# Kernel tuning notes

Measured on AMD Instinct MI355X. Metric: run time of the kernel, lower is better.

## Reference

```python
import jax, jax.numpy as jnp
import numpy as np

B, N, NKV = 2, 2048, 2048
E = 4096
H = 16
HD = E // H          # 256 head_dim
LQ = E // 8          # 512 q latent
LKV = E // 16        # 256 kv latent


def setup_inputs() -> dict:
    key = jax.random.key(0)
    ks = jax.random.split(key, 6)
    Q = jax.random.normal(ks[0], (B, N, E), dtype=jnp.float32)
    K = jax.random.normal(ks[1], (B, NKV, E), dtype=jnp.float32)
    # Linear weights stored as (in, out); scaled ~1/sqrt(fan_in) like torch default init
    Wq_d = jax.random.normal(ks[2], (E, LQ), dtype=jnp.float32) / np.sqrt(E)
    W_qk = jax.random.normal(ks[3], (LQ, H * LKV), dtype=jnp.float32) / np.sqrt(LQ)
    Wkv_d = jax.random.normal(ks[4], (E, LKV), dtype=jnp.float32) / np.sqrt(E)
    Wv_u = jax.random.normal(ks[5], (LKV, H * HD), dtype=jnp.float32) / np.sqrt(LKV)
    return {"Q": Q, "K": K, "Wq_d": Wq_d, "W_qk": W_qk, "Wkv_d": Wkv_d, "Wv_u": Wv_u}


def reference(Q, K, Wq_d, W_qk, Wkv_d, Wv_u):
    b, n, _ = Q.shape
    nkv = K.shape[1]
    C_q = Q @ Wq_d                                   # [B,N,Lq]
    C_kv = K @ Wkv_d                                 # [B,Nkv,Lkv]
    CqWqk = (C_q @ W_qk).reshape(b, n, H, LKV)       # [B,N,H,Lkv]
    # scores contract over the kv latent dim (absorbed-weight MLA)
    scores = jnp.einsum('bnhl,bkl->bhnk', CqWqk, C_kv) / jnp.sqrt(
        jnp.asarray(LKV, dtype=Q.dtype))             # [B,H,N,Nkv]
    attn = jax.nn.softmax(scores, axis=-1)
    V_up = (C_kv @ Wv_u).reshape(b, nkv, H, HD)      # [B,Nkv,H,hd]
    out = jnp.einsum('bhnk,bkhd->bnhd', attn, V_up)  # [B,N,H,hd]
    return out.reshape(b, n, H * HD)                 # [B,N,E]
```

## Files before the change

kernel.cpp:

```cpp
#include <hip/hip_runtime.h>


#define B_ 2
#define N_ 2048
#define H_ 16
#define HD_ 256
#define LKV_ 256

typedef __attribute__((ext_vector_type(8))) short bf8;
typedef __attribute__((ext_vector_type(4))) float f4;
typedef __attribute__((ext_vector_type(4))) unsigned short us4v;
typedef unsigned short u16;

__device__ __forceinline__ u16 f2b(float f) {
  union { float f; unsigned u; } v; v.f = f;
  unsigned r = (v.u + 0x7FFFu + ((v.u >> 16) & 1u)) >> 16;
  return (u16)r;
}

__device__ __forceinline__ void load_lds16(const void* g, void* l) {
  __builtin_amdgcn_global_load_lds(
      (const __attribute__((address_space(1))) unsigned int*)(unsigned long long)(uintptr_t)g,
      (__attribute__((address_space(3))) unsigned int*)(unsigned int)(uintptr_t)l,
      16, 0, 0);
}

__global__ __launch_bounds__(256) void cvt_bf16(const float* __restrict__ src,
                                                u16* __restrict__ dst, int n4)
{
  int i = blockIdx.x * 256 + threadIdx.x;
  if (i < n4) {
    float4 v = *(const float4*)(src + (size_t)i * 4);
    us4v o = {f2b(v.x), f2b(v.y), f2b(v.z), f2b(v.w)};
    *(us4v*)(dst + (size_t)i * 4) = o;
  }
}

__global__ __launch_bounds__(256) void cvt_transpose(const float* __restrict__ src,
                                                     u16* __restrict__ dst, int R, int C)
{
  __shared__ float tile[32][33];
  const int t = threadIdx.x;
  const int tr = t & 31, tc = t >> 5;
  const int r0 = blockIdx.x * 32, c0 = blockIdx.y * 32;
#pragma unroll
  for (int i = 0; i < 4; ++i)
    tile[tc + i * 8][tr] = src[(size_t)(r0 + tc + i * 8) * C + c0 + tr];
  __syncthreads();
#pragma unroll
  for (int i = 0; i < 4; ++i)
    dst[(size_t)(c0 + tc + i * 8) * R + r0 + tr] = f2b(tile[tr][tc + i * 8]);
}

__global__ __launch_bounds__(256) void gemm_bt(
    const u16* __restrict__ A,
    const u16* __restrict__ Bt,
    u16* __restrict__ C,
    int M, int N, int K)
{
  __shared__ u16 As[128 * 32];
  __shared__ u16 Bs[128 * 32];

  const int t = threadIdx.x;
  const int w = t >> 6, lane = t & 63;
  const int quad = lane >> 4, l16 = lane & 15;
  const int n0 = blockIdx.x * 128, m0 = blockIdx.y * 128;
  const int wm = (w >> 1) * 64, wn = (w & 1) * 64;

  f4 acc[4][4];
#pragma unroll
  for (int mi = 0; mi < 4; ++mi)
#pragma unroll
    for (int ni = 0; ni < 4; ++ni) acc[mi][ni] = (f4){0.f, 0.f, 0.f, 0.f};

  const u16* Ap = A + (size_t)m0 * K;
  const u16* Bp = Bt + (size_t)n0 * K;
  const int srow = t >> 2, spos = (t & 3) * 8;

  for (int k0 = 0; k0 < K; k0 += 32) {
    __syncthreads();
    load_lds16(Ap + (size_t)srow * K + k0 + spos,        &As[(size_t)t * 8]);
    load_lds16(Ap + (size_t)(srow + 64) * K + k0 + spos, &As[(size_t)(256 + t) * 8]);
    load_lds16(Bp + (size_t)srow * K + k0 + spos,        &Bs[(size_t)t * 8]);
    load_lds16(Bp + (size_t)(srow + 64) * K + k0 + spos, &Bs[(size_t)(256 + t) * 8]);
    __syncthreads();

    bf8 af[4], bfr[4];
#pragma unroll
    for (int mi = 0; mi < 4; ++mi)
      af[mi] = *(const bf8*)(&As[(wm + mi * 16 + l16) * 32 + quad * 8]);
#pragma unroll
    for (int ni = 0; ni < 4; ++ni)
      bfr[ni] = *(const bf8*)(&Bs[(wn + ni * 16 + l16) * 32 + quad * 8]);
#pragma unroll
    for (int mi = 0; mi < 4; ++mi)
#pragma unroll
      for (int ni = 0; ni < 4; ++ni)
        acc[mi][ni] = __builtin_amdgcn_mfma_f32_16x16x32_bf16(af[mi], bfr[ni], acc[mi][ni], 0, 0, 0);
  }

  u16* Cp = C + (size_t)m0 * N + n0;
#pragma unroll
  for (int mi = 0; mi < 4; ++mi)
#pragma unroll
    for (int r = 0; r < 4; ++r) {
      int m = wm + mi * 16 + quad * 4 + r;
#pragma unroll
      for (int ni = 0; ni < 4; ++ni)
        Cp[(size_t)m * N + wn + ni * 16 + l16] = f2b(acc[mi][ni][r]);
    }
}

__global__ __launch_bounds__(256) void transpose_v(const u16* __restrict__ vupB,
                                                   u16* __restrict__ vupT)
{
  __shared__ u16 tile[64][78];
  const int t = threadIdx.x;
  const int key0 = blockIdx.x * 64, d0 = blockIdx.y * 64;
  const int bh = blockIdx.z, b = bh >> 4, h = bh & 15;

#pragma unroll
  for (int i = 0; i < 2; ++i) {
    int c = t + 256 * i;
    int key = c >> 3, d8 = c & 7;
    bf8 v = *(const bf8*)(vupB + ((size_t)(b * N_ + key0 + key) * (H_ * HD_)) + h * HD_ + d0 + d8 * 8);
    *(bf8*)(&tile[key][d8 * 8]) = v;
  }
  __syncthreads();
#pragma unroll
  for (int i = 0; i < 2; ++i) {
    int c = t + 256 * i;
    int d = c >> 3, k8 = c & 7;
    bf8 v;
#pragma unroll
    for (int j = 0; j < 8; ++j) v[j] = (short)tile[k8 * 8 + j][d];
    *(bf8*)(vupT + ((size_t)bh * HD_ + d0 + d) * (size_t)N_ + key0 + k8 * 8) = v;
  }
}

__global__ __launch_bounds__(256, 2) void flash_mfma(
    const u16* __restrict__ q2b,
    const u16* __restrict__ ckvb,
    const u16* __restrict__ vupT,
    float* __restrict__ out)
{
  __shared__ u16 KtL[32 * 264];
  __shared__ u16 VtL[256 * 40];
  __shared__ u16 PtL[128 * 40];

  const int t = threadIdx.x;
  const int w = t >> 6, lane = t & 63;
  const int quad = lane >> 4, l16 = lane & 15;
  const int n0 = blockIdx.x * 128;
  const int bh = blockIdx.y, b = bh >> 4, h = bh & 15;

  bf8 qf[2][8];
  {
    const u16* qbase = q2b + (size_t)(b * N_ + n0 + w * 32 + l16) * (H_ * LKV_) + h * LKV_ + quad * 8;
#pragma unroll
    for (int mi = 0; mi < 2; ++mi)
#pragma unroll
      for (int ks = 0; ks < 8; ++ks)
        qf[mi][ks] = *(const bf8*)(qbase + (size_t)(mi * 16) * (H_ * LKV_) + ks * 32);
  }

  f4 o[2][16];
#pragma unroll
  for (int mi = 0; mi < 2; ++mi)
#pragma unroll
    for (int dt = 0; dt < 16; ++dt) o[mi][dt] = (f4){0.f, 0.f, 0.f, 0.f};
  float ms[2][4], ls[2][4];
#pragma unroll
  for (int mi = 0; mi < 2; ++mi)
#pragma unroll
    for (int r = 0; r < 4; ++r) { ms[mi][r] = -1e30f; ls[mi][r] = 0.f; }

  const u16* kgb = ckvb + (size_t)b * N_ * LKV_;
  const u16* vgb = vupT + (size_t)bh * HD_ * N_;

  for (int k0 = 0; k0 < N_; k0 += 32) {
    __syncthreads();
#pragma unroll
    for (int i = 0; i < 4; ++i) {
      int c = t + 256 * i;
      int key = c >> 5, l8 = c & 31;
      bf8 v = *(const bf8*)(kgb + (size_t)(k0 + key) * LKV_ + l8 * 8);
      *(bf8*)(&KtL[key * 264 + l8 * 8]) = v;
    }
#pragma unroll
    for (int i = 0; i < 4; ++i) {
      int c = t + 256 * i;
      int d = c >> 2, k8 = c & 3;
      bf8 v = *(const bf8*)(vgb + (size_t)d * N_ + k0 + k8 * 8);
      *(bf8*)(&VtL[d * 40 + k8 * 8]) = v;
    }
    __syncthreads();

    f4 sf[2][2];
    sf[0][0] = (f4){0,0,0,0}; sf[0][1] = (f4){0,0,0,0};
    sf[1][0] = (f4){0,0,0,0}; sf[1][1] = (f4){0,0,0,0};
#pragma unroll
    for (int nt = 0; nt < 2; ++nt) {
      const u16* kr = &KtL[(nt * 16 + l16) * 264 + quad * 8];
#pragma unroll
      for (int ks = 0; ks < 8; ++ks) {
        bf8 kf = *(const bf8*)(kr + ks * 32);
        sf[0][nt] = __builtin_amdgcn_mfma_f32_16x16x32_bf16(qf[0][ks], kf, sf[0][nt], 0, 0, 0);
        sf[1][nt] = __builtin_amdgcn_mfma_f32_16x16x32_bf16(qf[1][ks], kf, sf[1][nt], 0, 0, 0);
      }
    }

#pragma unroll
    for (int mi = 0; mi < 2; ++mi) {
      float al[4];
#pragma unroll
      for (int r = 0; r < 4; ++r) {
        float a0 = sf[mi][0][r] * 0.0625f;
        float a1 = sf[mi][1][r] * 0.0625f;
        float mx = fmaxf(a0, a1);
#pragma unroll
        for (int off = 1; off < 16; off <<= 1) mx = fmaxf(mx, __shfl_xor(mx, off, 16));
        float mn = fmaxf(ms[mi][r], mx);
        float p0 = __expf(a0 - mn), p1 = __expf(a1 - mn);
        float sum = p0 + p1;
#pragma unroll
        for (int off = 1; off < 16; off <<= 1) sum += __shfl_xor(sum, off, 16);
        al[r] = __expf(ms[mi][r] - mn);
        ls[mi][r] = ls[mi][r] * al[r] + sum;
        ms[mi][r] = mn;
        int q = w * 32 + mi * 16 + quad * 4 + r;
        PtL[q * 40 + l16]      = f2b(p0);
        PtL[q * 40 + 16 + l16] = f2b(p1);
      }
#pragma unroll
      for (int dt = 0; dt < 16; ++dt) {
        o[mi][dt][0] *= al[0]; o[mi][dt][1] *= al[1];
        o[mi][dt][2] *= al[2]; o[mi][dt][3] *= al[3];
      }
    }
    __syncthreads();

    bf8 pf0 = *(const bf8*)(&PtL[(w * 32 + l16) * 40 + quad * 8]);
    bf8 pf1 = *(const bf8*)(&PtL[(w * 32 + 16 + l16) * 40 + quad * 8]);
#pragma unroll
    for (int dt = 0; dt < 16; ++dt) {
      bf8 vf = *(const bf8*)(&VtL[(dt * 16 + l16) * 40 + quad * 8]);
      o[0][dt] = __builtin_amdgcn_mfma_f32_16x16x32_bf16(pf0, vf, o[0][dt], 0, 0, 0);
      o[1][dt] = __builtin_amdgcn_mfma_f32_16x16x32_bf16(pf1, vf, o[1][dt], 0, 0, 0);
    }
  }

#pragma unroll
  for (int mi = 0; mi < 2; ++mi)
#pragma unroll
    for (int r = 0; r < 4; ++r) {
      float iv = 1.f / ls[mi][r];
      float* dst = out + (size_t)(b * N_ + n0 + w * 32 + mi * 16 + quad * 4 + r) * (H_ * HD_)
                   + h * HD_ + l16;
#pragma unroll
      for (int dt = 0; dt < 16; ++dt) dst[dt * 16] = o[mi][dt][r] * iv;
    }
}

extern "C" void kernel_launch(void* const* d_in, const int* in_sizes, int n_in,
                              void* d_out, int out_size, void* d_ws, size_t ws_size,
                              hipStream_t stream) {
  const float* Q     = (const float*)d_in[0];
  const float* Kin   = (const float*)d_in[1];
  const float* Wq_d  = (const float*)d_in[2];
  const float* W_qk  = (const float*)d_in[3];
  const float* Wkv_d = (const float*)d_in[4];
  const float* Wv_u  = (const float*)d_in[5];
  float* out = (float*)d_out;

  char* ws = (char*)d_ws;
  u16* qbf   = (u16*)(ws);
  u16* vupT  = qbf;
  u16* kbf   = (u16*)(ws + 33554432);
  u16* vupB  = kbf;
  u16* q2b   = (u16*)(ws + 67108864);
  u16* cqb   = (u16*)(ws + 100663296);
  u16* ckvb  = (u16*)(ws + 104857600);
  u16* wqdT  = (u16*)(ws + 106954752);
  u16* wqkT  = (u16*)(ws + 111149056);
  u16* wkvdT = (u16*)(ws + 115343360);
  u16* wvuT  = (u16*)(ws + 117440512);

  cvt_bf16<<<dim3(16384), 256, 0, stream>>>(Q,   qbf, 4194304);
  cvt_bf16<<<dim3(16384), 256, 0, stream>>>(Kin, kbf, 4194304);
  cvt_transpose<<<dim3(128, 16), 256, 0, stream>>>(Wq_d,  wqdT,  4096, 512);
  cvt_transpose<<<dim3(16, 128), 256, 0, stream>>>(W_qk,  wqkT,  512, 4096);
  cvt_transpose<<<dim3(128, 8),  256, 0, stream>>>(Wkv_d, wkvdT, 4096, 256);
  cvt_transpose<<<dim3(8, 128),  256, 0, stream>>>(Wv_u,  wvuT,  256, 4096);

  gemm_bt<<<dim3(4, 32), 256, 0, stream>>>(qbf, wqdT, cqb, 4096, 512, 4096);
  gemm_bt<<<dim3(2, 32), 256, 0, stream>>>(kbf, wkvdT, ckvb, 4096, 256, 4096);
  gemm_bt<<<dim3(32, 32), 256, 0, stream>>>(cqb, wqkT, q2b, 4096, 4096, 512);
  gemm_bt<<<dim3(32, 32), 256, 0, stream>>>(ckvb, wvuT, vupB, 4096, 4096, 256);
  transpose_v<<<dim3(32, 4, 32), 256, 0, stream>>>(vupB, vupT);
  flash_mfma<<<dim3(16, 32), 256, 0, stream>>>(q2b, ckvb, vupT, out);
}
```

Measured before the change: 790.5 us.

## Read K/V fragments directly from global in flash kernel; merge down-projection launches

```diff
diff --git a/kernel.cpp b/kernel.cpp
--- a/kernel.cpp
+++ b/kernel.cpp
@@ -25,15 +25,17 @@
       16, 0, 0);
 }
 
-__global__ __launch_bounds__(256) void cvt_bf16(const float* __restrict__ src,
-                                                u16* __restrict__ dst, int n4)
+__global__ __launch_bounds__(256) void cvt_bf16_2(const float* __restrict__ a,
+                                                  u16* __restrict__ da,
+                                                  const float* __restrict__ b,
+                                                  u16* __restrict__ db, int n4)
 {
   int i = blockIdx.x * 256 + threadIdx.x;
-  if (i < n4) {
-    float4 v = *(const float4*)(src + (size_t)i * 4);
-    us4v o = {f2b(v.x), f2b(v.y), f2b(v.z), f2b(v.w)};
-    *(us4v*)(dst + (size_t)i * 4) = o;
-  }
+  const float* s; u16* d;
+  if (i < n4) { s = a; d = da; } else { s = b; d = db; i -= n4; }
+  float4 v = *(const float4*)(s + (size_t)i * 4);
+  us4v o = {f2b(v.x), f2b(v.y), f2b(v.z), f2b(v.w)};
+  *(us4v*)(d + (size_t)i * 4) = o;
 }
 
 __global__ __launch_bounds__(256) void cvt_transpose(const float* __restrict__ src,
@@ -111,6 +113,67 @@
     }
 }
 
+__global__ __launch_bounds__(256) void gemm_qkv(
+    const u16* __restrict__ Aq, const u16* __restrict__ Bq, u16* __restrict__ Cq,
+    const u16* __restrict__ Ak, const u16* __restrict__ Bk, u16* __restrict__ Ck)
+{
+  const int K = 4096;
+  __shared__ u16 As[128 * 32];
+  __shared__ u16 Bs[64 * 32];
+
+  const u16* A; const u16* Bt; u16* C; int N, n0;
+  if (blockIdx.x < 8) { A = Aq; Bt = Bq; C = Cq; N = 512; n0 = blockIdx.x * 64; }
+  else               { A = Ak; Bt = Bk; C = Ck; N = 256; n0 = (blockIdx.x - 8) * 64; }
+
+  const int t = threadIdx.x;
+  const int w = t >> 6, lane = t & 63;
+  const int quad = lane >> 4, l16 = lane & 15;
+  const int m0 = blockIdx.y * 128;
+  const int wm = (w >> 1) * 64, wn = (w & 1) * 32;
+
+  f4 acc[4][2];
+#pragma unroll
+  for (int mi = 0; mi < 4; ++mi)
+#pragma unroll
+    for (int ni = 0; ni < 2; ++ni) acc[mi][ni] = (f4){0.f, 0.f, 0.f, 0.f};
+
+  const u16* Ap = A + (size_t)m0 * K;
+  const u16* Bp = Bt + (size_t)n0 * K;
+  const int srow = t >> 2, spos = (t & 3) * 8;
+
+  for (int k0 = 0; k0 < K; k0 += 32) {
+    __syncthreads();
+    load_lds16(Ap + (size_t)srow * K + k0 + spos,        &As[(size_t)t * 8]);
+    load_lds16(Ap + (size_t)(srow + 64) * K + k0 + spos, &As[(size_t)(256 + t) * 8]);
+    load_lds16(Bp + (size_t)srow * K + k0 + spos,        &Bs[(size_t)t * 8]);
+    __syncthreads();
+
+    bf8 af[4], bfr[2];
+#pragma unroll
+    for (int mi = 0; mi < 4; ++mi)
+      af[mi] = *(const bf8*)(&As[(wm + mi * 16 + l16) * 32 + quad * 8]);
+#pragma unroll
+    for (int ni = 0; ni < 2; ++ni)
+      bfr[ni] = *(const bf8*)(&Bs[(wn + ni * 16 + l16) * 32 + quad * 8]);
+#pragma unroll
+    for (int mi = 0; mi < 4; ++mi)
+#pragma unroll
+      for (int ni = 0; ni < 2; ++ni)
+        acc[mi][ni] = __builtin_amdgcn_mfma_f32_16x16x32_bf16(af[mi], bfr[ni], acc[mi][ni], 0, 0, 0);
+  }
+
+  u16* Cp = C + (size_t)m0 * N + n0;
+#pragma unroll
+  for (int mi = 0; mi < 4; ++mi)
+#pragma unroll
+    for (int r = 0; r < 4; ++r) {
+      int m = wm + mi * 16 + quad * 4 + r;
+#pragma unroll
+      for (int ni = 0; ni < 2; ++ni)
+        Cp[(size_t)m * N + wn + ni * 16 + l16] = f2b(acc[mi][ni][r]);
+    }
+}
+
 __global__ __launch_bounds__(256) void transpose_v(const u16* __restrict__ vupB,
                                                    u16* __restrict__ vupT)
 {
@@ -144,8 +207,6 @@
     const u16* __restrict__ vupT,
     float* __restrict__ out)
 {
-  __shared__ u16 KtL[32 * 264];
-  __shared__ u16 VtL[256 * 40];
   __shared__ u16 PtL[128 * 40];
 
   const int t = threadIdx.x;
@@ -175,33 +236,16 @@
 #pragma unroll
     for (int r = 0; r < 4; ++r) { ms[mi][r] = -1e30f; ls[mi][r] = 0.f; }
 
-  const u16* kgb = ckvb + (size_t)b * N_ * LKV_;
-  const u16* vgb = vupT + (size_t)bh * HD_ * N_;
+  const u16* kgb = ckvb + (size_t)b * N_ * LKV_ + quad * 8;
+  const u16* vgb = vupT + (size_t)bh * HD_ * N_ + (size_t)l16 * N_ + quad * 8;
 
   for (int k0 = 0; k0 < N_; k0 += 32) {
-    __syncthreads();
-#pragma unroll
-    for (int i = 0; i < 4; ++i) {
-      int c = t + 256 * i;
-      int key = c >> 5, l8 = c & 31;
-      bf8 v = *(const bf8*)(kgb + (size_t)(k0 + key) * LKV_ + l8 * 8);
-      *(bf8*)(&KtL[key * 264 + l8 * 8]) = v;
-    }
-#pragma unroll
-    for (int i = 0; i < 4; ++i) {
-      int c = t + 256 * i;
-      int d = c >> 2, k8 = c & 3;
-      bf8 v = *(const bf8*)(vgb + (size_t)d * N_ + k0 + k8 * 8);
-      *(bf8*)(&VtL[d * 40 + k8 * 8]) = v;
-    }
-    __syncthreads();
-
     f4 sf[2][2];
     sf[0][0] = (f4){0,0,0,0}; sf[0][1] = (f4){0,0,0,0};
     sf[1][0] = (f4){0,0,0,0}; sf[1][1] = (f4){0,0,0,0};
 #pragma unroll
     for (int nt = 0; nt < 2; ++nt) {
-      const u16* kr = &KtL[(nt * 16 + l16) * 264 + quad * 8];
+      const u16* kr = kgb + (size_t)(k0 + nt * 16 + l16) * LKV_;
 #pragma unroll
       for (int ks = 0; ks < 8; ++ks) {
         bf8 kf = *(const bf8*)(kr + ks * 32);
@@ -238,15 +282,21 @@
         o[mi][dt][2] *= al[2]; o[mi][dt][3] *= al[3];
       }
     }
-    __syncthreads();
 
     bf8 pf0 = *(const bf8*)(&PtL[(w * 32 + l16) * 40 + quad * 8]);
     bf8 pf1 = *(const bf8*)(&PtL[(w * 32 + 16 + l16) * 40 + quad * 8]);
+
+    const u16* vr = vgb + k0;
+    bf8 vf[8];
+#pragma unroll
+    for (int j = 0; j < 8; ++j)
+      vf[j] = *(const bf8*)(vr + (size_t)(j * 16) * N_);
 #pragma unroll
     for (int dt = 0; dt < 16; ++dt) {
-      bf8 vf = *(const bf8*)(&VtL[(dt * 16 + l16) * 40 + quad * 8]);
-      o[0][dt] = __builtin_amdgcn_mfma_f32_16x16x32_bf16(pf0, vf, o[0][dt], 0, 0, 0);
-      o[1][dt] = __builtin_amdgcn_mfma_f32_16x16x32_bf16(pf1, vf, o[1][dt], 0, 0, 0);
+      bf8 cur = vf[dt & 7];
+      if (dt < 8) vf[dt & 7] = *(const bf8*)(vr + (size_t)((dt + 8) * 16) * N_);
+      o[0][dt] = __builtin_amdgcn_mfma_f32_16x16x32_bf16(pf0, cur, o[0][dt], 0, 0, 0);
+      o[1][dt] = __builtin_amdgcn_mfma_f32_16x16x32_bf16(pf1, cur, o[1][dt], 0, 0, 0);
     }
   }
 
@@ -286,15 +336,13 @@
   u16* wkvdT = (u16*)(ws + 115343360);
   u16* wvuT  = (u16*)(ws + 117440512);
 
-  cvt_bf16<<<dim3(16384), 256, 0, stream>>>(Q,   qbf, 4194304);
-  cvt_bf16<<<dim3(16384), 256, 0, stream>>>(Kin, kbf, 4194304);
+  cvt_bf16_2<<<dim3(32768), 256, 0, stream>>>(Q, qbf, Kin, kbf, 4194304);
   cvt_transpose<<<dim3(128, 16), 256, 0, stream>>>(Wq_d,  wqdT,  4096, 512);
   cvt_transpose<<<dim3(16, 128), 256, 0, stream>>>(W_qk,  wqkT,  512, 4096);
   cvt_transpose<<<dim3(128, 8),  256, 0, stream>>>(Wkv_d, wkvdT, 4096, 256);
   cvt_transpose<<<dim3(8, 128),  256, 0, stream>>>(Wv_u,  wvuT,  256, 4096);
 
-  gemm_bt<<<dim3(4, 32), 256, 0, stream>>>(qbf, wqdT, cqb, 4096, 512, 4096);
-  gemm_bt<<<dim3(2, 32), 256, 0, stream>>>(kbf, wkvdT, ckvb, 4096, 256, 4096);
+  gemm_qkv<<<dim3(12, 32), 256, 0, stream>>>(qbf, wqdT, cqb, kbf, wkvdT, ckvb);
   gemm_bt<<<dim3(32, 32), 256, 0, stream>>>(cqb, wqkT, q2b, 4096, 4096, 512);
   gemm_bt<<<dim3(32, 32), 256, 0, stream>>>(ckvb, wvuT, vupB, 4096, 4096, 256);
   transpose_v<<<dim3(32, 4, 32), 256, 0, stream>>>(vupB, vupT);
```

New measurement: 924.2 us. +16.9%, slower.
